# Kernel optimization log

Hardware: AMD Instinct MI355X
Metric: run time of the kernel (lower is better)

## Reference

```python
import jax, jax.numpy as jnp
import numpy as np

B, L, D, K, MAXL = 2, 1024, 256, 64, 1024
EPS = 1e-5

def _encode(x, pos, w1, b1, w2, b2, wa, ba):
    # x: [B,L,D] -> complex phasors [B,L,K]
    xa = x + pos[: x.shape[1]][None]
    h = jax.nn.gelu(xa @ w1 + b1, approximate=False)
    phase = jnp.tanh(h @ w2 + b2) * np.float32(np.pi)
    amp = jax.nn.softplus(xa @ wa + ba) + np.float32(0.1)
    return (amp * jnp.exp(1j * phase)).astype(jnp.complex64)

def setup_inputs() -> dict:
    key = jax.random.key(0)
    ks = jax.random.split(key, 24)
    def lin_w(k, i, o):
        return (jax.random.normal(k, (i, o), jnp.float32) / np.sqrt(np.float32(i)))
    def pos(k):
        return jax.random.normal(k, (MAXL, D), jnp.float32) * np.float32(0.02)
    inp = {
        'x': jax.random.normal(ks[0], (B, L, D), jnp.float32),
        'pos_k': pos(ks[1]),
        'w1_k': lin_w(ks[2], D, D), 'b1_k': jnp.zeros((D,), jnp.float32),
        'w2_k': lin_w(ks[3], D, K), 'b2_k': jnp.zeros((K,), jnp.float32),
        'wa_k': lin_w(ks[4], D, K), 'ba_k': jnp.zeros((K,), jnp.float32),
        'pos_q': pos(ks[5]),
        'w1_q': lin_w(ks[6], D, D), 'b1_q': jnp.zeros((D,), jnp.float32),
        'w2_q': lin_w(ks[7], D, K), 'b2_q': jnp.zeros((K,), jnp.float32),
        'wa_q': lin_w(ks[8], D, K), 'ba_q': jnp.zeros((K,), jnp.float32),
        'wv': lin_w(ks[9], D, D), 'bv': jnp.zeros((D,), jnp.float32),
        'ln_g': jnp.ones((D,), jnp.float32), 'ln_b': jnp.zeros((D,), jnp.float32),
        'wo': lin_w(ks[10], D, D), 'bo': jnp.zeros((D,), jnp.float32),
    }
    return inp

def reference(x, pos_k, w1_k, b1_k, w2_k, b2_k, wa_k, ba_k,
              pos_q, w1_q, b1_q, w2_q, b2_q, wa_q, ba_q,
              wv, bv, ln_g, ln_b, wo, bo):
    Bx, Lx, Dx = x.shape
    kp = _encode(x, pos_k, w1_k, b1_k, w2_k, b2_k, wa_k, ba_k)  # [B,L,K] complex
    qp = _encode(x, pos_q, w1_q, b1_q, w2_q, b2_q, wa_q, ba_q)  # [B,L,K] complex
    V = (x @ wv + bv).astype(jnp.complex64)                      # [B,L,D]
    bound = kp[:, :, :, None] * V[:, :, None, :]                 # [B,L,K,D]
    memory = jnp.cumsum(bound, axis=1)                           # [B,L,K,D]
    retrieved = jnp.real(jnp.einsum('blkd,blk->bld', memory, jnp.conj(qp)))
    positions = jnp.arange(1, Lx + 1, dtype=jnp.float32)
    norm = jnp.sqrt(positions * np.float32(kp.shape[-1]))[None, :, None]
    r = retrieved / norm
    mu = jnp.mean(r, axis=-1, keepdims=True)
    var = jnp.var(r, axis=-1, keepdims=True)
    rn = (r - mu) / jnp.sqrt(var + np.float32(EPS)) * ln_g + ln_b
    return x + rn @ wo + bo
```

## Files before the change

### kernel.cpp

```cpp
#include <hip/hip_runtime.h>
#include <hip/hip_bf16.h>

typedef __attribute__((ext_vector_type(8))) short short8;
typedef __attribute__((ext_vector_type(4))) float float4v;

constexpr int B = 2, L = 1024, D = 256, K = 64;
constexpr int N = B * L;
constexpr int NC = L / 64;

constexpr int WT2_OFF = 524288;

__device__ __forceinline__ ushort bf16_hi(float v) {
  return (ushort)(__float_as_uint(v) >> 16);
}
__device__ __forceinline__ float hi_f(float v) {
  return __uint_as_float(__float_as_uint(v) & 0xFFFF0000u);
}
__device__ __forceinline__ ushort bf16_rne(float v) {
  uint b = __float_as_uint(v);
  b += 0x7FFF + ((b >> 16) & 1);
  return (ushort)(b >> 16);
}

__global__ __launch_bounds__(256) void prep_kernel(
    const float* __restrict__ w1_k, const float* __restrict__ w1_q,
    const float* __restrict__ wv, const float* __restrict__ wo,
    const float* __restrict__ w2_k, const float* __restrict__ wa_k,
    const float* __restrict__ w2_q, const float* __restrict__ wa_q,
    ushort* __restrict__ WT) {
  __shared__ float Lt[64][65];
  const int bi = blockIdx.x, tid = threadIdx.x;
  const float* src;
  int ncols, k0, n0;
  ushort* dhi;
  int losz;
  if (bi < 64) {
    const int m = bi >> 4, t = bi & 15;
    src = (m == 0) ? w1_k : (m == 1) ? w1_q : (m == 2) ? wv : wo;
    ncols = 256; k0 = (t >> 2) * 64; n0 = (t & 3) * 64;
    dhi = WT + m * 131072; losz = 65536;
  } else {
    const int m = (bi - 64) >> 2, kt = (bi - 64) & 3;
    src = (m == 0) ? w2_k : (m == 1) ? wa_k : (m == 2) ? w2_q : wa_q;
    ncols = 64; k0 = kt * 64; n0 = 0;
    dhi = WT + WT2_OFF + m * 32768; losz = 16384;
  }
  ushort* dlo = dhi + losz;
  for (int p = 0; p < 16; ++p) {
    const int kr = p * 4 + (tid >> 6), nc = tid & 63;
    Lt[kr][nc] = src[(k0 + kr) * ncols + n0 + nc];
  }
  __syncthreads();
  const int n = tid >> 2, kq = tid & 3;
  uint uh[8], ul[8];
  for (int i = 0; i < 8; ++i) {
    const float v0 = Lt[kq * 16 + 2 * i][n];
    const float v1 = Lt[kq * 16 + 2 * i + 1][n];
    uh[i] = (uint)bf16_hi(v0) | ((uint)bf16_hi(v1) << 16);
    ul[i] = (uint)bf16_rne(v0 - hi_f(v0)) | ((uint)bf16_rne(v1 - hi_f(v1)) << 16);
  }
  const int oidx = (n0 + n) * 256 + k0 + kq * 16;
  *(uint4*)&dhi[oidx] = make_uint4(uh[0], uh[1], uh[2], uh[3]);
  *(uint4*)&dhi[oidx + 8] = make_uint4(uh[4], uh[5], uh[6], uh[7]);
  *(uint4*)&dlo[oidx] = make_uint4(ul[0], ul[1], ul[2], ul[3]);
  *(uint4*)&dlo[oidx + 8] = make_uint4(ul[4], ul[5], ul[6], ul[7]);
}

__global__ __launch_bounds__(256) void enc1_kernel(
    const float* __restrict__ x, const float* __restrict__ pos_k,
    const float* __restrict__ pos_q,
    const float* __restrict__ b1_k, const float* __restrict__ b1_q,
    const float* __restrict__ bv, const ushort* __restrict__ WT,
    float* __restrict__ hk, float* __restrict__ hq, float* __restrict__ V) {
  __shared__ __align__(16) ushort Ah[32][40], Al[32][40];
  __shared__ __align__(16) ushort Bh[128][40], Bl[128][40];
  const int tid = threadIdx.x;
  const int g = blockIdx.x / 128;
  const int rem = blockIdx.x % 128;
  const int row0 = (rem >> 1) * 32, nb = (rem & 1) * 128;
  const float* pos = (g == 0) ? pos_k : (g == 1) ? pos_q : nullptr;
  const ushort* Wh = WT + g * 131072;
  const ushort* Wl = Wh + 65536;
  const int w = tid >> 6, lane = tid & 63;
  const int m16 = lane & 15, quad = lane >> 4;

  float4v acc[2][2] = {};

  for (int k0 = 0; k0 < 256; k0 += 32) {
    __syncthreads();
    {
      const int r = tid >> 3, kc = (tid & 7) * 4;
      const int row = row0 + r, l = row & (L - 1);
      float4 xv = *(const float4*)&x[row * D + k0 + kc];
      if (pos) {
        const float4 pv = *(const float4*)&pos[l * D + k0 + kc];
        xv.x += pv.x; xv.y += pv.y; xv.z += pv.z; xv.w += pv.w;
      }
      ushort4 h4, l4;
      h4.x = bf16_hi(xv.x); l4.x = bf16_rne(xv.x - hi_f(xv.x));
      h4.y = bf16_hi(xv.y); l4.y = bf16_rne(xv.y - hi_f(xv.y));
      h4.z = bf16_hi(xv.z); l4.z = bf16_rne(xv.z - hi_f(xv.z));
      h4.w = bf16_hi(xv.w); l4.w = bf16_rne(xv.w - hi_f(xv.w));
      *(ushort4*)&Ah[r][kc] = h4;
      *(ushort4*)&Al[r][kc] = l4;
    }
#pragma unroll
    for (int p = 0; p < 2; ++p) {
      const int n = (tid >> 2) + p * 64, chunk = tid & 3;
      const int ga = (nb + n) * 256 + k0 + chunk * 8;
      *(uint4*)&Bh[n][chunk * 8] = *(const uint4*)&Wh[ga];
      *(uint4*)&Bl[n][chunk * 8] = *(const uint4*)&Wl[ga];
    }
    __syncthreads();

    short8 afh[2], afl[2], bfh[2], bfl[2];
#pragma unroll
    for (int r = 0; r < 2; ++r) {
      afh[r] = *(const short8*)&Ah[r * 16 + m16][quad * 8];
      afl[r] = *(const short8*)&Al[r * 16 + m16][quad * 8];
    }
#pragma unroll
    for (int c = 0; c < 2; ++c) {
      const int col = w * 32 + c * 16 + m16;
      bfh[c] = *(const short8*)&Bh[col][quad * 8];
      bfl[c] = *(const short8*)&Bl[col][quad * 8];
    }
#pragma unroll
    for (int r = 0; r < 2; ++r)
#pragma unroll
      for (int c = 0; c < 2; ++c) {
        acc[r][c] = __builtin_amdgcn_mfma_f32_16x16x32_bf16(afh[r], bfh[c], acc[r][c], 0, 0, 0);
        acc[r][c] = __builtin_amdgcn_mfma_f32_16x16x32_bf16(afh[r], bfl[c], acc[r][c], 0, 0, 0);
        acc[r][c] = __builtin_amdgcn_mfma_f32_16x16x32_bf16(afl[r], bfh[c], acc[r][c], 0, 0, 0);
      }
  }

  float* outp = (g == 0) ? hk : (g == 1) ? hq : V;
  const float* bp = (g == 0) ? b1_k : (g == 1) ? b1_q : bv;
#pragma unroll
  for (int c = 0; c < 2; ++c) {
    const int colg = nb + w * 32 + c * 16 + m16;
    const float bias = bp[colg];
#pragma unroll
    for (int r = 0; r < 2; ++r)
#pragma unroll
      for (int j = 0; j < 4; ++j) {
        const int rowg = row0 + r * 16 + quad * 4 + j;
        float v = acc[r][c][j] + bias;
        if (g < 2) v = 0.5f * v * (1.0f + erff(v * 0.70710678f));
        outp[rowg * D + colg] = v;
      }
  }
}

__global__ __launch_bounds__(512) void enc2_kernel(
    const float* __restrict__ x, const float* __restrict__ pos_k,
    const float* __restrict__ pos_q, const float* __restrict__ hk,
    const float* __restrict__ hq,
    const float* __restrict__ b2_k, const float* __restrict__ ba_k,
    const float* __restrict__ b2_q, const float* __restrict__ ba_q,
    const ushort* __restrict__ WT,
    float* __restrict__ kr, float* __restrict__ ki,
    float* __restrict__ qr, float* __restrict__ qi) {
  __shared__ __align__(16) ushort Ahh[16][40], Ahl[16][40], Axh[16][40], Axl[16][40];
  __shared__ __align__(16) ushort B2h[64][40], B2l[64][40], Bah[64][40], Bal[64][40];
  __shared__ float phL[16][68], amL[16][68];
  const int tid = threadIdx.x;
  const int e = blockIdx.x >> 7;
  const int r0g = (blockIdx.x & 127) * 16;
  const float* hsrc = e ? hq : hk;
  const float* pos = e ? pos_q : pos_k;
  const ushort* W2h = WT + WT2_OFF + (e ? 2 : 0) * 32768;
  const ushort* W2l = W2h + 16384;
  const ushort* Wah = WT + WT2_OFF + (e ? 3 : 1) * 32768;
  const ushort* Wal = Wah + 16384;
  const int w = tid >> 6, lane = tid & 63;
  const int m16 = lane & 15, quad = lane >> 4;
  const int mat = w & 1, ct = w >> 1;

  float4v acc = {};
  for (int k0 = 0; k0 < 256; k0 += 32) {
    __syncthreads();
    {
      const int half = tid >> 8;
      const int t2 = tid & 255;
      const int r = t2 >> 4, kc = (t2 & 15) * 2;
      const int row = r0g + r, l = row & (L - 1);
      if (half == 0) {
        const float2 hv = *(const float2*)&hsrc[row * D + k0 + kc];
        ushort2 h2, l2;
        h2.x = bf16_hi(hv.x); l2.x = bf16_rne(hv.x - hi_f(hv.x));
        h2.y = bf16_hi(hv.y); l2.y = bf16_rne(hv.y - hi_f(hv.y));
        *(ushort2*)&Ahh[r][kc] = h2;
        *(ushort2*)&Ahl[r][kc] = l2;
      } else {
        const float2 xv = *(const float2*)&x[row * D + k0 + kc];
        const float2 pv = *(const float2*)&pos[l * D + k0 + kc];
        const float a0 = xv.x + pv.x, a1 = xv.y + pv.y;
        ushort2 h2, l2;
        h2.x = bf16_hi(a0); l2.x = bf16_rne(a0 - hi_f(a0));
        h2.y = bf16_hi(a1); l2.y = bf16_rne(a1 - hi_f(a1));
        *(ushort2*)&Axh[r][kc] = h2;
        *(ushort2*)&Axl[r][kc] = l2;
      }
    }
    {
      const int sel = tid >> 7;
      const int idx = tid & 127;
      const int n = idx >> 1, ch = (idx & 1) * 2;
      const int ga = n * 256 + k0 + ch * 8;
      const ushort* s = (sel == 0) ? W2h : (sel == 1) ? W2l : (sel == 2) ? Wah : Wal;
      ushort* dst = (sel == 0) ? &B2h[n][ch * 8] : (sel == 1) ? &B2l[n][ch * 8]
                  : (sel == 2) ? &Bah[n][ch * 8] : &Bal[n][ch * 8];
      *(uint4*)dst = *(const uint4*)&s[ga];
      *(uint4*)(dst + 8) = *(const uint4*)&s[ga + 8];
    }
    __syncthreads();

    const short8 ah = mat ? *(const short8*)&Axh[m16][quad * 8]
                          : *(const short8*)&Ahh[m16][quad * 8];
    const short8 al = mat ? *(const short8*)&Axl[m16][quad * 8]
                          : *(const short8*)&Ahl[m16][quad * 8];
    const int col = ct * 16 + m16;
    const short8 bh = mat ? *(const short8*)&Bah[col][quad * 8]
                          : *(const short8*)&B2h[col][quad * 8];
    const short8 bl = mat ? *(const short8*)&Bal[col][quad * 8]
                          : *(const short8*)&B2l[col][quad * 8];
    acc = __builtin_amdgcn_mfma_f32_16x16x32_bf16(ah, bh, acc, 0, 0, 0);
    acc = __builtin_amdgcn_mfma_f32_16x16x32_bf16(ah, bl, acc, 0, 0, 0);
    acc = __builtin_amdgcn_mfma_f32_16x16x32_bf16(al, bh, acc, 0, 0, 0);
  }

  {
    const int colk = ct * 16 + m16;
    if (mat == 0) {
      const float b2v = (e ? b2_q : b2_k)[colk];
#pragma unroll
      for (int j = 0; j < 4; ++j)
        phL[quad * 4 + j][colk] = tanhf(acc[j] + b2v) * 3.14159265358979f;
    } else {
      const float bav = (e ? ba_q : ba_k)[colk];
#pragma unroll
      for (int j = 0; j < 4; ++j) {
        const float av = acc[j] + bav;
        amL[quad * 4 + j][colk] = fmaxf(av, 0.0f) + log1pf(expf(-fabsf(av))) + 0.1f;
      }
    }
  }
  __syncthreads();
  {
    float* pr = e ? qr : kr;
    float* pim = e ? qi : ki;
#pragma unroll
    for (int p = 0; p < 2; ++p) {
      const int idx = p * 512 + tid;
      const int r = idx >> 6, ccol = idx & 63;
      const int row = r0g + r;
      const float a = amL[r][ccol], pph = phL[r][ccol];
      pr[row * K + ccol] = a * cosf(pph);
      pim[row * K + ccol] = a * sinf(pph);
    }
  }
}

__global__ __launch_bounds__(256) void tbuild_kernel(
    const float* __restrict__ kr, const float* __restrict__ ki,
    const float* __restrict__ V, float* __restrict__ TMt) {
  const int id = blockIdx.x;
  const int dc = id & 15, c = (id >> 4) & 15, b = id >> 8;
  const int tid = threadIdx.x;
  const int n0 = b * L + c * 64;
  const int dl = tid & 15;
  const int d = dc * 16 + dl;
  const int kb = tid >> 4;

  __shared__ float krL[64][68], kiL[64][68];
  __shared__ float Tl[16][200];
  for (int e = tid; e < 1024; e += 256) {
    const int t = e >> 4, k4 = (e & 15) * 4;
    *(float4*)&krL[t][k4] = *(const float4*)&kr[(n0 + t) * K + k4];
    *(float4*)&kiL[t][k4] = *(const float4*)&ki[(n0 + t) * K + k4];
  }
  __syncthreads();

  float vcol[64];
#pragma unroll 8
  for (int t = 0; t < 64; ++t) vcol[t] = V[(n0 + t) * D + d];

  float ar[4] = {0.f, 0.f, 0.f, 0.f}, ai[4] = {0.f, 0.f, 0.f, 0.f};
#pragma unroll 4
  for (int t = 0; t < 64; ++t) {
    const float vt = vcol[t];
    const float4 k4r = *(const float4*)&krL[t][kb * 4];
    const float4 k4i = *(const float4*)&kiL[t][kb * 4];
    ar[0] += k4r.x * vt; ar[1] += k4r.y * vt; ar[2] += k4r.z * vt; ar[3] += k4r.w * vt;
    ai[0] += k4i.x * vt; ai[1] += k4i.y * vt; ai[2] += k4i.z * vt; ai[3] += k4i.w * vt;
  }

#pragma unroll
  for (int i = 0; i < 4; ++i) {
    Tl[dl][kb * 4 + i] = ar[i];
    Tl[dl][64 + kb * 4 + i] = ai[i];
  }
  if (kb == 0) {
#pragma unroll
    for (int j = 0; j < 16; ++j) Tl[dl][128 + j] = vcol[j];
  } else if (kb == 1) {
#pragma unroll
    for (int j = 0; j < 16; ++j) Tl[dl][144 + j] = vcol[16 + j];
  } else if (kb == 2) {
#pragma unroll
    for (int j = 0; j < 16; ++j) Tl[dl][160 + j] = vcol[32 + j];
  } else if (kb == 3) {
#pragma unroll
    for (int j = 0; j < 16; ++j) Tl[dl][176 + j] = vcol[48 + j];
  }
  __syncthreads();

  float* dst = &TMt[(((size_t)(b * 16 + c)) * 256 + dc * 16) * 192];
#pragma unroll
  for (int p = 0; p < 3; ++p) {
    const int e = p * 256 + tid;
    const int row = e / 48, f4 = e % 48;
    *(float4*)&dst[(size_t)row * 192 + f4 * 4] = *(const float4*)&Tl[row][f4 * 4];
  }
}

__global__ __launch_bounds__(256) void scan_kernel(float* __restrict__ TMt) {
  const int col = blockIdx.x * 256 + threadIdx.x;
  const int b = col >> 15;
  const int d = (col >> 7) & 255;
  const int inner = col & 127;
  size_t idx = (((size_t)(b * 16)) * 256 + d) * 192 + inner;
  const size_t stride = (size_t)256 * 192;
  float run = 0.f;
#pragma unroll
  for (int c = 0; c < NC; ++c, idx += stride) {
    const float t = TMt[idx];
    TMt[idx] = run;
    run += t;
  }
}

__global__ __launch_bounds__(512) void ret_kernel(
    const float* __restrict__ qr, const float* __restrict__ qi,
    const float* __restrict__ kr, const float* __restrict__ ki,
    const float* __restrict__ TMt, float* __restrict__ ret,
    float* __restrict__ LNred) {
  __shared__ __align__(16) ushort Ah[64][200], Al[64][200];
  __shared__ __align__(16) ushort Kh[64][136], Kl[64][136];
  __shared__ __align__(16) ushort Bh[32][200], Bl[32][200];
  const int tid = threadIdx.x;
  const int dc = blockIdx.x & 7;
  const int c = (blockIdx.x >> 3) & 15;
  const int b = blockIdx.x >> 7;
  const int n0 = b * L + c * 64;
  const int cols0 = dc * 32;
  const int w = tid >> 6, lane = tid & 63;
  const int m16 = lane & 15, quad = lane >> 4;

#pragma unroll
  for (int j = 0; j < 4; ++j) {
    const int e = j * 512 + tid;
    const int row = e >> 5, c4 = e & 31;
    const int col0 = (c4 & 15) * 4;
    const int acol = (c4 < 16 ? 0 : 64) + col0;
    {
      const float* src = (c4 < 16) ? qr : qi;
      const float4 v = *(const float4*)&src[(n0 + row) * K + col0];
      ushort4 h4, l4;
      h4.x = bf16_hi(v.x); l4.x = bf16_rne(v.x - hi_f(v.x));
      h4.y = bf16_hi(v.y); l4.y = bf16_rne(v.y - hi_f(v.y));
      h4.z = bf16_hi(v.z); l4.z = bf16_rne(v.z - hi_f(v.z));
      h4.w = bf16_hi(v.w); l4.w = bf16_rne(v.w - hi_f(v.w));
      *(ushort4*)&Ah[row][acol] = h4;
      *(ushort4*)&Al[row][acol] = l4;
    }
    {
      const float* src = (c4 < 16) ? kr : ki;
      const float4 v = *(const float4*)&src[(n0 + row) * K + col0];
      ushort4 h4, l4;
      h4.x = bf16_hi(v.x); l4.x = bf16_rne(v.x - hi_f(v.x));
      h4.y = bf16_hi(v.y); l4.y = bf16_rne(v.y - hi_f(v.y));
      h4.z = bf16_hi(v.z); l4.z = bf16_rne(v.z - hi_f(v.z));
      h4.w = bf16_hi(v.w); l4.w = bf16_rne(v.w - hi_f(v.w));
      *(ushort4*)&Kh[row][acol] = h4;
      *(ushort4*)&Kl[row][acol] = l4;
    }
  }
  __syncthreads();

  {
    const int rt = w & 3;
    const int cp = (w >> 2) * 2;
    float4v sc[2] = {};
#pragma unroll
    for (int kk = 0; kk < 128; kk += 32) {
      const short8 ah = *(const short8*)&Ah[rt * 16 + m16][kk + quad * 8];
      const short8 al = *(const short8*)&Al[rt * 16 + m16][kk + quad * 8];
#pragma unroll
      for (int cc = 0; cc < 2; ++cc) {
        const int ct = cp + cc;
        const short8 bh = *(const short8*)&Kh[ct * 16 + m16][kk + quad * 8];
        const short8 bl = *(const short8*)&Kl[ct * 16 + m16][kk + quad * 8];
        sc[cc] = __builtin_amdgcn_mfma_f32_16x16x32_bf16(ah, bh, sc[cc], 0, 0, 0);
        sc[cc] = __builtin_amdgcn_mfma_f32_16x16x32_bf16(ah, bl, sc[cc], 0, 0, 0);
        sc[cc] = __builtin_amdgcn_mfma_f32_16x16x32_bf16(al, bh, sc[cc], 0, 0, 0);
      }
    }
#pragma unroll
    for (int cc = 0; cc < 2; ++cc)
#pragma unroll
      for (int j = 0; j < 4; ++j) {
        const int row = rt * 16 + quad * 4 + j;
        const int t = (cp + cc) * 16 + m16;
        const float s = (t <= row) ? sc[cc][j] : 0.0f;
        Ah[row][128 + t] = bf16_hi(s);
        Al[row][128 + t] = bf16_rne(s - hi_f(s));
      }
  }

  {
    const float* src = &TMt[(((size_t)(b * 16 + c)) * 256 + cols0) * 192];
#pragma unroll
    for (int p = 0; p < 3; ++p) {
      const int e = p * 512 + tid;
      const int row = e / 48, f4 = e % 48;
      const float4 v = *(const float4*)&src[(size_t)row * 192 + f4 * 4];
      ushort4 h4, l4;
      h4.x = bf16_hi(v.x); l4.x = bf16_rne(v.x - hi_f(v.x));
      h4.y = bf16_hi(v.y); l4.y = bf16_rne(v.y - hi_f(v.y));
      h4.z = bf16_hi(v.z); l4.z = bf16_rne(v.z - hi_f(v.z));
      h4.w = bf16_hi(v.w); l4.w = bf16_rne(v.w - hi_f(v.w));
      *(ushort4*)&Bh[row][f4 * 4] = h4;
      *(ushort4*)&Bl[row][f4 * 4] = l4;
    }
  }
  __syncthreads();

  {
    const int rt = w & 3;
    const int ct = w >> 2;
    float4v r2 = {};
#pragma unroll
    for (int kk = 0; kk < 6; ++kk) {
      const short8 ah = *(const short8*)&Ah[rt * 16 + m16][kk * 32 + quad * 8];
      const short8 al = *(const short8*)&Al[rt * 16 + m16][kk * 32 + quad * 8];
      const short8 bh = *(const short8*)&Bh[ct * 16 + m16][kk * 32 + quad * 8];
      const short8 bl = *(const short8*)&Bl[ct * 16 + m16][kk * 32 + quad * 8];
      r2 = __builtin_amdgcn_mfma_f32_16x16x32_bf16(ah, bh, r2, 0, 0, 0);
      r2 = __builtin_amdgcn_mfma_f32_16x16x32_bf16(ah, bl, r2, 0, 0, 0);
      r2 = __builtin_amdgcn_mfma_f32_16x16x32_bf16(al, bh, r2, 0, 0, 0);
    }
#pragma unroll
    for (int j = 0; j < 4; ++j) {
      const int rowL = rt * 16 + quad * 4 + j;
      const float nrm = rsqrtf((float)(c * 64 + rowL + 1) * 64.0f);
      const float v = r2[j] * nrm;
      ret[(size_t)(n0 + rowL) * D + cols0 + ct * 16 + m16] = v;
      float sj = v, s2j = v * v;
      for (int off = 1; off < 16; off <<= 1) {
        sj += __shfl_xor(sj, off, 64);
        s2j += __shfl_xor(s2j, off, 64);
      }
      if (m16 == 0) {
        LNred[(size_t)(n0 + rowL) * 32 + (dc * 2 + ct) * 2 + 0] = sj;
        LNred[(size_t)(n0 + rowL) * 32 + (dc * 2 + ct) * 2 + 1] = s2j;
      }
    }
  }
}

__global__ __launch_bounds__(512) void out2_kernel(
    const float* __restrict__ ret, const float* __restrict__ LNred,
    const float* __restrict__ x, const float* __restrict__ ln_g,
    const float* __restrict__ ln_b, const ushort* __restrict__ WT,
    const float* __restrict__ bo, float* __restrict__ out) {
  __shared__ __align__(16) ushort Ah[32][40], Al[32][40];
  __shared__ __align__(16) ushort Bh[64][40], Bl[64][40];
  __shared__ float mu_s[32], rs_s[32];
  const int tid = threadIdx.x;
  const int row0 = (blockIdx.x >> 2) * 32, nb = (blockIdx.x & 3) * 64;
  const ushort* Wh = WT + 3 * 131072;
  const ushort* Wl = Wh + 65536;
  const int w = tid >> 6, lane = tid & 63;
  const int m16 = lane & 15, quad = lane >> 4;
  const int rt = w & 1, cq = w >> 1;

  if (tid < 32) {
    const int row = row0 + tid;
    float s = 0.f, s2 = 0.f;
#pragma unroll
    for (int i = 0; i < 16; ++i) {
      s += LNred[(size_t)row * 32 + i * 2 + 0];
      s2 += LNred[(size_t)row * 32 + i * 2 + 1];
    }
    const float mu = s * (1.0f / 256.0f);
    mu_s[tid] = mu;
    rs_s[tid] = rsqrtf(s2 * (1.0f / 256.0f) - mu * mu + 1e-5f);
  }

  float4v acc = {};
  for (int k0 = 0; k0 < 256; k0 += 32) {
    __syncthreads();
    {
      const int r = tid >> 4, kc = (tid & 15) * 2;
      const float2 v = *(const float2*)&ret[(size_t)(row0 + r) * D + k0 + kc];
      const float2 g2 = *(const float2*)&ln_g[k0 + kc];
      const float2 b2 = *(const float2*)&ln_b[k0 + kc];
      const float mu = mu_s[r], rs = rs_s[r];
      const float a0 = (v.x - mu) * rs * g2.x + b2.x;
      const float a1 = (v.y - mu) * rs * g2.y + b2.y;
      ushort2 h2, l2;
      h2.x = bf16_hi(a0); l2.x = bf16_rne(a0 - hi_f(a0));
      h2.y = bf16_hi(a1); l2.y = bf16_rne(a1 - hi_f(a1));
      *(ushort2*)&Ah[r][kc] = h2;
      *(ushort2*)&Al[r][kc] = l2;
    }
    {
      const int plane = tid >> 8;
      const int n = (tid >> 2) & 63, chunk = tid & 3;
      const int ga = (nb + n) * 256 + k0 + chunk * 8;
      if (plane == 0) *(uint4*)&Bh[n][chunk * 8] = *(const uint4*)&Wh[ga];
      else            *(uint4*)&Bl[n][chunk * 8] = *(const uint4*)&Wl[ga];
    }
    __syncthreads();

    const short8 afh = *(const short8*)&Ah[rt * 16 + m16][quad * 8];
    const short8 afl = *(const short8*)&Al[rt * 16 + m16][quad * 8];
    const int col = cq * 16 + m16;
    const short8 bfh = *(const short8*)&Bh[col][quad * 8];
    const short8 bfl = *(const short8*)&Bl[col][quad * 8];
    acc = __builtin_amdgcn_mfma_f32_16x16x32_bf16(afh, bfh, acc, 0, 0, 0);
    acc = __builtin_amdgcn_mfma_f32_16x16x32_bf16(afh, bfl, acc, 0, 0, 0);
    acc = __builtin_amdgcn_mfma_f32_16x16x32_bf16(afl, bfh, acc, 0, 0, 0);
  }

  const int colg = nb + cq * 16 + m16;
  const float bias = bo[colg];
#pragma unroll
  for (int j = 0; j < 4; ++j) {
    const int rowg = row0 + rt * 16 + quad * 4 + j;
    out[rowg * D + colg] = x[rowg * D + colg] + acc[j] + bias;
  }
}

extern "C" void kernel_launch(void* const* d_in, const int* in_sizes, int n_in,
                              void* d_out, int out_size, void* d_ws, size_t ws_size,
                              hipStream_t stream) {
  (void)in_sizes; (void)n_in; (void)out_size; (void)ws_size;
  const float* x    = (const float*)d_in[0];
  const float* pos_k= (const float*)d_in[1];
  const float* w1_k = (const float*)d_in[2];
  const float* b1_k = (const float*)d_in[3];
  const float* w2_k = (const float*)d_in[4];
  const float* b2_k = (const float*)d_in[5];
  const float* wa_k = (const float*)d_in[6];
  const float* ba_k = (const float*)d_in[7];
  const float* pos_q= (const float*)d_in[8];
  const float* w1_q = (const float*)d_in[9];
  const float* b1_q = (const float*)d_in[10];
  const float* w2_q = (const float*)d_in[11];
  const float* b2_q = (const float*)d_in[12];
  const float* wa_q = (const float*)d_in[13];
  const float* ba_q = (const float*)d_in[14];
  const float* wv   = (const float*)d_in[15];
  const float* bv   = (const float*)d_in[16];
  const float* ln_g = (const float*)d_in[17];
  const float* ln_b = (const float*)d_in[18];
  const float* wo   = (const float*)d_in[19];
  const float* bo   = (const float*)d_in[20];

  float* ws = (float*)d_ws;
  float* kr = ws;
  float* ki = kr + (size_t)N * K;
  float* qr = ki + (size_t)N * K;
  float* qi = qr + (size_t)N * K;
  float* V  = qi + (size_t)N * K;
  float* TMt = V + (size_t)N * D;
  float* ret = TMt + (size_t)B * NC * 256 * 192;
  float* LNred = ret + (size_t)N * D;
  float* hk = LNred + (size_t)N * 32;
  float* hq = hk + (size_t)N * D;
  ushort* WT = (ushort*)(hq + (size_t)N * D);

  prep_kernel<<<80, 256, 0, stream>>>(w1_k, w1_q, wv, wo,
                                      w2_k, wa_k, w2_q, wa_q, WT);
  enc1_kernel<<<384, 256, 0, stream>>>(x, pos_k, pos_q, b1_k, b1_q, bv, WT,
                                       hk, hq, V);
  enc2_kernel<<<256, 512, 0, stream>>>(x, pos_k, pos_q, hk, hq,
                                       b2_k, ba_k, b2_q, ba_q, WT,
                                       kr, ki, qr, qi);
  tbuild_kernel<<<B * NC * 16, 256, 0, stream>>>(kr, ki, V, TMt);
  scan_kernel<<<256, 256, 0, stream>>>(TMt);
  ret_kernel<<<B * NC * 8, 512, 0, stream>>>(qr, qi, kr, ki, TMt, ret, LNred);
  out2_kernel<<<256, 512, 0, stream>>>(ret, LNred, x, ln_g, ln_b, WT, bo,
                                       (float*)d_out);
}
```

Measured before the change: 160.2 us.

## Fold chunk prefix scan into retrieval kernel and stage V tile via shared memory

```diff
diff --git a/kernel.cpp b/kernel.cpp
--- a/kernel.cpp
+++ b/kernel.cpp
@@ -271,26 +271,32 @@
   const int tid = threadIdx.x;
   const int n0 = b * L + c * 64;
   const int dl = tid & 15;
-  const int d = dc * 16 + dl;
   const int kb = tid >> 4;
 
   __shared__ float krL[64][68], kiL[64][68];
-  __shared__ float Tl[16][200];
+  __shared__ float VL[64][20];
+  __shared__ float Tl[16][204];
   for (int e = tid; e < 1024; e += 256) {
     const int t = e >> 4, k4 = (e & 15) * 4;
     *(float4*)&krL[t][k4] = *(const float4*)&kr[(n0 + t) * K + k4];
     *(float4*)&kiL[t][k4] = *(const float4*)&ki[(n0 + t) * K + k4];
   }
+  {
+    const int t = tid >> 2, f = (tid & 3) * 4;
+    *(float4*)&VL[t][f] = *(const float4*)&V[(n0 + t) * D + dc * 16 + f];
+  }
   __syncthreads();
 
-  float vcol[64];
-#pragma unroll 8
-  for (int t = 0; t < 64; ++t) vcol[t] = V[(n0 + t) * D + d];
+  {
+    const int t0 = (tid >> 4) * 4;
+#pragma unroll
+    for (int i = 0; i < 4; ++i) Tl[dl][128 + t0 + i] = VL[t0 + i][dl];
+  }
 
   float ar[4] = {0.f, 0.f, 0.f, 0.f}, ai[4] = {0.f, 0.f, 0.f, 0.f};
 #pragma unroll 4
   for (int t = 0; t < 64; ++t) {
-    const float vt = vcol[t];
+    const float vt = VL[t][dl];
     const float4 k4r = *(const float4*)&krL[t][kb * 4];
     const float4 k4i = *(const float4*)&kiL[t][kb * 4];
     ar[0] += k4r.x * vt; ar[1] += k4r.y * vt; ar[2] += k4r.z * vt; ar[3] += k4r.w * vt;
@@ -302,19 +308,6 @@
     Tl[dl][kb * 4 + i] = ar[i];
     Tl[dl][64 + kb * 4 + i] = ai[i];
   }
-  if (kb == 0) {
-#pragma unroll
-    for (int j = 0; j < 16; ++j) Tl[dl][128 + j] = vcol[j];
-  } else if (kb == 1) {
-#pragma unroll
-    for (int j = 0; j < 16; ++j) Tl[dl][144 + j] = vcol[16 + j];
-  } else if (kb == 2) {
-#pragma unroll
-    for (int j = 0; j < 16; ++j) Tl[dl][160 + j] = vcol[32 + j];
-  } else if (kb == 3) {
-#pragma unroll
-    for (int j = 0; j < 16; ++j) Tl[dl][176 + j] = vcol[48 + j];
-  }
   __syncthreads();
 
   float* dst = &TMt[(((size_t)(b * 16 + c)) * 256 + dc * 16) * 192];
@@ -323,22 +316,6 @@
     const int e = p * 256 + tid;
     const int row = e / 48, f4 = e % 48;
     *(float4*)&dst[(size_t)row * 192 + f4 * 4] = *(const float4*)&Tl[row][f4 * 4];
-  }
-}
-
-__global__ __launch_bounds__(256) void scan_kernel(float* __restrict__ TMt) {
-  const int col = blockIdx.x * 256 + threadIdx.x;
-  const int b = col >> 15;
-  const int d = (col >> 7) & 255;
-  const int inner = col & 127;
-  size_t idx = (((size_t)(b * 16)) * 256 + d) * 192 + inner;
-  const size_t stride = (size_t)256 * 192;
-  float run = 0.f;
-#pragma unroll
-  for (int c = 0; c < NC; ++c, idx += stride) {
-    const float t = TMt[idx];
-    TMt[idx] = run;
-    run += t;
   }
 }
 
@@ -388,6 +365,20 @@
       *(ushort4*)&Kl[row][acol] = l4;
     }
   }
+
+  float4 mac0 = {}, mac1 = {};
+  {
+    const int prow = tid >> 4, in0 = (tid & 15) * 8;
+    const float* base = &TMt[(size_t)(b * 16) * 256 * 192 +
+                             (size_t)(cols0 + prow) * 192 + in0];
+    for (int cp = 0; cp < c; ++cp) {
+      const float* p = base + (size_t)cp * 256 * 192;
+      const float4 v0 = *(const float4*)p;
+      const float4 v1 = *(const float4*)(p + 4);
+      mac0.x += v0.x; mac0.y += v0.y; mac0.z += v0.z; mac0.w += v0.w;
+      mac1.x += v1.x; mac1.y += v1.y; mac1.z += v1.z; mac1.w += v1.w;
+    }
+  }
   __syncthreads();
 
   {
@@ -421,20 +412,31 @@
   }
 
   {
-    const float* src = &TMt[(((size_t)(b * 16 + c)) * 256 + cols0) * 192];
-#pragma unroll
-    for (int p = 0; p < 3; ++p) {
-      const int e = p * 512 + tid;
-      const int row = e / 48, f4 = e % 48;
-      const float4 v = *(const float4*)&src[(size_t)row * 192 + f4 * 4];
-      ushort4 h4, l4;
-      h4.x = bf16_hi(v.x); l4.x = bf16_rne(v.x - hi_f(v.x));
-      h4.y = bf16_hi(v.y); l4.y = bf16_rne(v.y - hi_f(v.y));
-      h4.z = bf16_hi(v.z); l4.z = bf16_rne(v.z - hi_f(v.z));
-      h4.w = bf16_hi(v.w); l4.w = bf16_rne(v.w - hi_f(v.w));
-      *(ushort4*)&Bh[row][f4 * 4] = h4;
-      *(ushort4*)&Bl[row][f4 * 4] = l4;
-    }
+    const int prow = tid >> 4, in0 = (tid & 15) * 8;
+    ushort4 h4, l4;
+    h4.x = bf16_hi(mac0.x); l4.x = bf16_rne(mac0.x - hi_f(mac0.x));
+    h4.y = bf16_hi(mac0.y); l4.y = bf16_rne(mac0.y - hi_f(mac0.y));
+    h4.z = bf16_hi(mac0.z); l4.z = bf16_rne(mac0.z - hi_f(mac0.z));
+    h4.w = bf16_hi(mac0.w); l4.w = bf16_rne(mac0.w - hi_f(mac0.w));
+    *(ushort4*)&Bh[prow][in0] = h4;
+    *(ushort4*)&Bl[prow][in0] = l4;
+    h4.x = bf16_hi(mac1.x); l4.x = bf16_rne(mac1.x - hi_f(mac1.x));
+    h4.y = bf16_hi(mac1.y); l4.y = bf16_rne(mac1.y - hi_f(mac1.y));
+    h4.z = bf16_hi(mac1.z); l4.z = bf16_rne(mac1.z - hi_f(mac1.z));
+    h4.w = bf16_hi(mac1.w); l4.w = bf16_rne(mac1.w - hi_f(mac1.w));
+    *(ushort4*)&Bh[prow][in0 + 4] = h4;
+    *(ushort4*)&Bl[prow][in0 + 4] = l4;
+
+    const int vrow = tid >> 4, vin = 128 + (tid & 15) * 4;
+    const float4 v = *(const float4*)&TMt[(size_t)(b * 16 + c) * 256 * 192 +
+                                          (size_t)(cols0 + vrow) * 192 + vin];
+    ushort4 vh, vl;
+    vh.x = bf16_hi(v.x); vl.x = bf16_rne(v.x - hi_f(v.x));
+    vh.y = bf16_hi(v.y); vl.y = bf16_rne(v.y - hi_f(v.y));
+    vh.z = bf16_hi(v.z); vl.z = bf16_rne(v.z - hi_f(v.z));
+    vh.w = bf16_hi(v.w); vl.w = bf16_rne(v.w - hi_f(v.w));
+    *(ushort4*)&Bh[vrow][vin] = vh;
+    *(ushort4*)&Bl[vrow][vin] = vl;
   }
   __syncthreads();
 
@@ -592,7 +594,6 @@
                                        b2_k, ba_k, b2_q, ba_q, WT,
                                        kr, ki, qr, qi);
   tbuild_kernel<<<B * NC * 16, 256, 0, stream>>>(kr, ki, V, TMt);
-  scan_kernel<<<256, 256, 0, stream>>>(TMt);
   ret_kernel<<<B * NC * 8, 512, 0, stream>>>(qr, qi, kr, ki, TMt, ret, LNred);
   out2_kernel<<<256, 512, 0, stream>>>(ret, LNred, x, ln_g, ln_b, WT, bo,
                                        (float*)d_out);
```

Measured after the change: 148.4 us. -7.3%, faster.
